# Optimization experiments

Measured on AMD Instinct MI355X. Metric: run time of the kernel, lower is better.

## Reference

```python
import jax, jax.numpy as jnp
import numpy as np

N_EMB = 1024
HEAD_SIZE = 64
BLOCK_SIZE = 2048
B, T = 8, 2048


def setup_inputs() -> dict:
    key = jax.random.key(0)
    kx, kq, kk, kv = jax.random.split(key, 4)
    scale = 1.0 / (N_EMB ** 0.5)
    x = jax.random.normal(kx, (B, T, N_EMB), dtype=jnp.float32)
    Wq = jax.random.uniform(kq, (N_EMB, HEAD_SIZE), dtype=jnp.float32) * scale
    Wk = jax.random.uniform(kk, (N_EMB, HEAD_SIZE), dtype=jnp.float32) * scale
    Wv = jax.random.uniform(kv, (N_EMB, HEAD_SIZE), dtype=jnp.float32) * scale
    return {"x": x, "Wq": Wq, "Wk": Wk, "Wv": Wv}


def reference(x, Wq, Wk, Wv):
    # Faithful to Head.__call__ with is_training=False.
    # NOTE: original code applies NO 1/sqrt(head_size) scaling to the scores.
    Bt, Tt, _ = x.shape
    q = x @ Wq                      # (B, T, H)
    k = x @ Wk                      # (B, T, H)
    v = x @ Wv                      # (B, T, H)
    wei = jnp.einsum('bth,bsh->bts', q, k)  # (B, T, T)
    causal = jnp.tril(jnp.ones((Tt, Tt), dtype=bool))
    wei = jnp.where(causal, wei, -jnp.inf)
    wei = jax.nn.softmax(wei, axis=-1)
    out = jnp.einsum('bts,bsh->bth', wei, v)  # (B, T, H)
    return out
```

## Files before the change

### kernel.cpp

```cpp
#include <hip/hip_runtime.h>
#include <hip/hip_bf16.h>

#define BB 8
#define TT 2048
#define EE 1024
#define HH 64

typedef __attribute__((ext_vector_type(8))) short short8;
typedef __attribute__((ext_vector_type(4))) float f32x4;

__device__ inline f32x4 mfma_16x16x32(short8 a, short8 b, f32x4 c) {
  return __builtin_amdgcn_mfma_f32_16x16x32_bf16(a, b, c, 0, 0, 0);
}

__device__ inline void gload_lds16(const __hip_bfloat16* g, __hip_bfloat16* l) {
  __builtin_amdgcn_global_load_lds((const __attribute__((address_space(1))) void*)g,
                                   (__attribute__((address_space(3))) void*)l,
                                   16, 0, 0);
}

__device__ inline short f2bf(float f) {
  __hip_bfloat16 h = __float2bfloat16(f);
  return *reinterpret_cast<short*>(&h);
}
__device__ inline float bf2f(short s) {
  __hip_bfloat16 h = *reinterpret_cast<__hip_bfloat16*>(&s);
  return __bfloat162float(h);
}

#define WAIT_LGKM0() __builtin_amdgcn_s_waitcnt(0xC07F)

__global__ void prep_w(const float* __restrict__ Wq, const float* __restrict__ Wk,
                       const float* __restrict__ Wv,
                       __hip_bfloat16* __restrict__ Wthi,
                       __hip_bfloat16* __restrict__ Wtlo) {
  const int n = blockIdx.x;
  const int m = n >> 6;
  const int h = n & 63;
  const float* W = (m == 0) ? Wq : (m == 1) ? Wk : Wv;
  const int e0 = threadIdx.x * 4;
#pragma unroll
  for (int j = 0; j < 4; ++j) {
    const float w = W[(e0 + j) * 64 + h];
    const __hip_bfloat16 hi = __float2bfloat16(w);
    Wthi[n * 1024 + e0 + j] = hi;
    Wtlo[n * 1024 + e0 + j] = __float2bfloat16(w - __bfloat162float(hi));
  }
}

__global__ __launch_bounds__(256) void qkv_gemm(
    const float* __restrict__ x,
    const __hip_bfloat16* __restrict__ Wthi, const __hip_bfloat16* __restrict__ Wtlo,
    __hip_bfloat16* __restrict__ qhi, __hip_bfloat16* __restrict__ qlo,
    __hip_bfloat16* __restrict__ khi, __hip_bfloat16* __restrict__ klo,
    __hip_bfloat16* __restrict__ vT) {
  __shared__ __hip_bfloat16 Ahi[2][64 * 72];
  __shared__ __hip_bfloat16 Alo[2][64 * 72];
  __shared__ __hip_bfloat16 Bhi[2][192 * 64];
  __shared__ __hip_bfloat16 Blo[2][128 * 64];

  const int tid  = threadIdx.x;
  const int wave = tid >> 6;
  const int lane = tid & 63;
  const int row0 = blockIdx.x * 64;

  const int lr = tid >> 2;
  const int le = (tid & 3) * 16;
  const float* xrow = x + (row0 + lr) * 1024 + le;

  f32x4 acc[12];
#pragma unroll
  for (int j = 0; j < 12; ++j) acc[j] = f32x4{0.f, 0.f, 0.f, 0.f};

  const int l15 = lane & 15, l4 = lane >> 4;

  auto issue_B = [&](int c, int buf) {
    const int g = (lane & 7) ^ ((lane >> 3) & 7);
#pragma unroll
    for (int s = 0; s < 6; ++s) {
      const int qq = wave * 6 + s;
      const int n  = qq * 8 + (lane >> 3);
      gload_lds16(Wthi + n * 1024 + c * 64 + g * 8, &Bhi[buf][qq * 512]);
      if (qq < 16)
        gload_lds16(Wtlo + n * 1024 + c * 64 + g * 8, &Blo[buf][qq * 512]);
    }
  };
  auto write_A = [&](int buf, const f32x4* xr) {
    short8 h0, h1, l0, l1;
    const float* xf = (const float*)xr;
#pragma unroll
    for (int j = 0; j < 8; ++j) {
      const float v = xf[j];
      const short h = f2bf(v);
      h0[j] = h;
      l0[j] = f2bf(v - bf2f(h));
    }
#pragma unroll
    for (int j = 0; j < 8; ++j) {
      const float v = xf[8 + j];
      const short h = f2bf(v);
      h1[j] = h;
      l1[j] = f2bf(v - bf2f(h));
    }
    *(short8*)&Ahi[buf][lr * 72 + le]     = h0;
    *(short8*)&Ahi[buf][lr * 72 + le + 8] = h1;
    *(short8*)&Alo[buf][lr * 72 + le]     = l0;
    *(short8*)&Alo[buf][lr * 72 + le + 8] = l1;
  };
  auto compute = [&](int buf) {
    const int tr = wave * 16 + l15;
    short8 ah0 = *(const short8*)&Ahi[buf][tr * 72 + l4 * 8];
    short8 ah1 = *(const short8*)&Ahi[buf][tr * 72 + 32 + l4 * 8];
    short8 al0 = *(const short8*)&Alo[buf][tr * 72 + l4 * 8];
    short8 al1 = *(const short8*)&Alo[buf][tr * 72 + 32 + l4 * 8];
#pragma unroll
    for (int j = 0; j < 12; ++j) {
      const int n  = j * 16 + l15;
      const int o0 = ((l4)     ^ (n & 7)) * 8;
      const int o1 = ((4 + l4) ^ (n & 7)) * 8;
      short8 bh0 = *(const short8*)&Bhi[buf][n * 64 + o0];
      short8 bh1 = *(const short8*)&Bhi[buf][n * 64 + o1];
      acc[j] = mfma_16x16x32(ah0, bh0, acc[j]);
      acc[j] = mfma_16x16x32(ah1, bh1, acc[j]);
      if (j < 8) {
        short8 bl0 = *(const short8*)&Blo[buf][n * 64 + o0];
        short8 bl1 = *(const short8*)&Blo[buf][n * 64 + o1];
        acc[j] = mfma_16x16x32(ah0, bl0, acc[j]);
        acc[j] = mfma_16x16x32(ah1, bl1, acc[j]);
        acc[j] = mfma_16x16x32(al0, bh0, acc[j]);
        acc[j] = mfma_16x16x32(al1, bh1, acc[j]);
      }
    }
  };

  f32x4 xr[4], xn[4];
  {
    const f32x4* p = (const f32x4*)xrow;
    xr[0] = p[0]; xr[1] = p[1]; xr[2] = p[2]; xr[3] = p[3];
  }
  issue_B(0, 0);
  __builtin_amdgcn_s_waitcnt(0);
  write_A(0, xr);
  __syncthreads();

  for (int c = 0; c < 16; ++c) {
    const int p = c & 1;
    if (c < 15) {
      const f32x4* pp = (const f32x4*)(xrow + (c + 1) * 64);
      xn[0] = pp[0]; xn[1] = pp[1]; xn[2] = pp[2]; xn[3] = pp[3];
      issue_B(c + 1, p ^ 1);
    }
    compute(p);
    if (c < 15) {
      __builtin_amdgcn_s_waitcnt(0);
      write_A(p ^ 1, xn);
    }
    __syncthreads();
  }

  const int strip = wave * 16;
#pragma unroll
  for (int j = 0; j < 12; ++j) {
    const int n  = j * 16 + l15;
    const int mm = n >> 6;
    const int h  = n & 63;
#pragma unroll
    for (int r = 0; r < 4; ++r) {
      const int trow = row0 + strip + l4 * 4 + r;
      const float val = acc[j][r];
      const __hip_bfloat16 hi = __float2bfloat16(val);
      const __hip_bfloat16 lo = __float2bfloat16(val - __bfloat162float(hi));
      if (mm == 0) {
        qhi[trow * 64 + h] = hi;
        qlo[trow * 64 + h] = lo;
      } else if (mm == 1) {
        khi[trow * 64 + h] = hi;
        klo[trow * 64 + h] = lo;
      } else {
        const int bb = trow >> 11, tl = trow & 2047;
        vT[(bb * 64 + h) * 2048 + tl] = hi;
      }
    }
  }
}

__global__ __launch_bounds__(256, 2) void attn(
    const __hip_bfloat16* __restrict__ qhi, const __hip_bfloat16* __restrict__ qlo,
    const __hip_bfloat16* __restrict__ khi, const __hip_bfloat16* __restrict__ klo,
    const __hip_bfloat16* __restrict__ vT, float* __restrict__ out) {
  __shared__ __hip_bfloat16 Psm[4][2][16 * 72];
  __shared__ float Osm[4][32][65];
  __shared__ float Msm[4][32];
  __shared__ float Lsm[4][32];

  const int tid  = threadIdx.x;
  const int wave = tid >> 6;
  const int lane = tid & 63;
  const int l15 = lane & 15, l4 = lane >> 4;

  const int b  = blockIdx.x & 7;
  const int ss = 63 - (blockIdx.x >> 3);
  const int t0 = ss * 32;
  const int ntiles = (ss >> 1) + 1;

  short8 qh0[2], qh1[2], ql0[2], ql1[2];
#pragma unroll
  for (int m = 0; m < 2; ++m) {
    const __hip_bfloat16* qph = qhi + (b * 2048 + t0 + m * 16 + l15) * 64;
    const __hip_bfloat16* qpl = qlo + (b * 2048 + t0 + m * 16 + l15) * 64;
    qh0[m] = *(const short8*)(qph + l4 * 8);
    qh1[m] = *(const short8*)(qph + 32 + l4 * 8);
    ql0[m] = *(const short8*)(qpl + l4 * 8);
    ql1[m] = *(const short8*)(qpl + 32 + l4 * 8);
  }

  f32x4 acc[2][4];
#pragma unroll
  for (int m = 0; m < 2; ++m)
#pragma unroll
    for (int j = 0; j < 4; ++j) acc[m][j] = f32x4{0.f, 0.f, 0.f, 0.f};
  float m_[2][4], l_[2][4];
#pragma unroll
  for (int m = 0; m < 2; ++m)
#pragma unroll
    for (int r = 0; r < 4; ++r) { m_[m][r] = -1e30f; l_[m][r] = 0.f; }

  const __hip_bfloat16* kbase_h = khi + (size_t)b * 2048 * 64;
  const __hip_bfloat16* kbase_l = klo + (size_t)b * 2048 * 64;
  const __hip_bfloat16* vbase   = vT + (size_t)b * 64 * 2048;

  for (int kt = wave; kt < ntiles; kt += 4) {
    const int k0 = kt << 6;
    const bool diag = (kt == ntiles - 1);

    short8 kh0[4], kh1[4], kl0[4], kl1[4];
#pragma unroll
    for (int j = 0; j < 4; ++j) {
      const __hip_bfloat16* kph = kbase_h + (k0 + j * 16 + l15) * 64;
      const __hip_bfloat16* kpl = kbase_l + (k0 + j * 16 + l15) * 64;
      kh0[j] = *(const short8*)(kph + l4 * 8);
      kh1[j] = *(const short8*)(kph + 32 + l4 * 8);
      kl0[j] = *(const short8*)(kpl + l4 * 8);
      kl1[j] = *(const short8*)(kpl + 32 + l4 * 8);
    }

#pragma unroll
    for (int m = 0; m < 2; ++m) {
      const int rowbase = t0 + m * 16;
      f32x4 s_[4];
#pragma unroll
      for (int j = 0; j < 4; ++j) {
        if (diag && (k0 + j * 16) > (rowbase + 15)) {
          s_[j] = f32x4{-1e30f, -1e30f, -1e30f, -1e30f};
          continue;
        }
        f32x4 z = f32x4{0.f, 0.f, 0.f, 0.f};
        z = mfma_16x16x32(qh0[m], kh0[j], z);
        z = mfma_16x16x32(qh1[m], kh1[j], z);
        z = mfma_16x16x32(qh0[m], kl0[j], z);
        z = mfma_16x16x32(qh1[m], kl1[j], z);
        z = mfma_16x16x32(ql0[m], kh0[j], z);
        z = mfma_16x16x32(ql1[m], kh1[j], z);
        s_[j] = z;
      }
      if (diag) {
#pragma unroll
        for (int j = 0; j < 4; ++j) {
          const int key = k0 + j * 16 + l15;
#pragma unroll
          for (int r = 0; r < 4; ++r) {
            const int row = rowbase + l4 * 4 + r;
            if (key > row) s_[j][r] = -1e30f;
          }
        }
      }

      float mx[4], rs[4], al[4];
#pragma unroll
      for (int r = 0; r < 4; ++r)
        mx[r] = fmaxf(fmaxf(s_[0][r], s_[1][r]), fmaxf(s_[2][r], s_[3][r]));
      for (int off = 1; off < 16; off <<= 1) {
#pragma unroll
        for (int r = 0; r < 4; ++r) mx[r] = fmaxf(mx[r], __shfl_xor(mx[r], off));
      }
#pragma unroll
      for (int r = 0; r < 4; ++r) {
        const float mn = fmaxf(m_[m][r], mx[r]);
        al[r] = __expf(m_[m][r] - mn);
        m_[m][r] = mn;
        rs[r] = 0.f;
      }
#pragma unroll
      for (int j = 0; j < 4; ++j) {
#pragma unroll
        for (int r = 0; r < 4; ++r) {
          const float pv = __expf(s_[j][r] - m_[m][r]);
          s_[j][r] = pv;
          rs[r] += pv;
        }
      }
      for (int off = 1; off < 16; off <<= 1) {
#pragma unroll
        for (int r = 0; r < 4; ++r) rs[r] += __shfl_xor(rs[r], off);
      }
#pragma unroll
      for (int r = 0; r < 4; ++r) l_[m][r] = l_[m][r] * al[r] + rs[r];
#pragma unroll
      for (int j = 0; j < 4; ++j)
#pragma unroll
        for (int r = 0; r < 4; ++r) acc[m][j][r] *= al[r];

#pragma unroll
      for (int j = 0; j < 4; ++j)
#pragma unroll
        for (int r = 0; r < 4; ++r)
          Psm[wave][m][(l4 * 4 + r) * 72 + j * 16 + l15] =
              __float2bfloat16(s_[j][r]);
    }

    short8 vf0[4], vf1[4];
#pragma unroll
    for (int j = 0; j < 4; ++j) {
      const __hip_bfloat16* vp = vbase + (j * 16 + l15) * 2048 + k0;
      vf0[j] = *(const short8*)(vp + l4 * 8);
      vf1[j] = *(const short8*)(vp + 32 + l4 * 8);
    }

    WAIT_LGKM0();

#pragma unroll
    for (int m = 0; m < 2; ++m) {
      short8 pf0 = *(const short8*)&Psm[wave][m][l15 * 72 + l4 * 8];
      short8 pf1 = *(const short8*)&Psm[wave][m][l15 * 72 + 32 + l4 * 8];
#pragma unroll
      for (int j = 0; j < 4; ++j) {
        acc[m][j] = mfma_16x16x32(pf0, vf0[j], acc[m][j]);
        acc[m][j] = mfma_16x16x32(pf1, vf1[j], acc[m][j]);
      }
    }
  }

#pragma unroll
  for (int m = 0; m < 2; ++m) {
#pragma unroll
    for (int j = 0; j < 4; ++j)
#pragma unroll
      for (int r = 0; r < 4; ++r)
        Osm[wave][m * 16 + l4 * 4 + r][j * 16 + l15] = acc[m][j][r];
    if (l15 == 0) {
#pragma unroll
      for (int r = 0; r < 4; ++r) {
        Msm[wave][m * 16 + l4 * 4 + r] = m_[m][r];
        Lsm[wave][m * 16 + l4 * 4 + r] = l_[m][r];
      }
    }
  }
  __syncthreads();

#pragma unroll
  for (int rr = 0; rr < 8; ++rr) {
    const int row = wave * 8 + rr;
    float M = fmaxf(fmaxf(Msm[0][row], Msm[1][row]),
                    fmaxf(Msm[2][row], Msm[3][row]));
    float L = 0.f, O = 0.f;
#pragma unroll
    for (int w2 = 0; w2 < 4; ++w2) {
      const float a = __expf(Msm[w2][row] - M);
      L += a * Lsm[w2][row];
      O += a * Osm[w2][row][lane];
    }
    out[(b * 2048 + t0 + row) * 64 + lane] = O / L;
  }
}

extern "C" void kernel_launch(void* const* d_in, const int* in_sizes, int n_in,
                              void* d_out, int out_size, void* d_ws, size_t ws_size,
                              hipStream_t stream) {
  const float* x  = (const float*)d_in[0];
  const float* Wq = (const float*)d_in[1];
  const float* Wk = (const float*)d_in[2];
  const float* Wv = (const float*)d_in[3];
  float* out = (float*)d_out;

  char* ws = (char*)d_ws;
  __hip_bfloat16* Wthi = (__hip_bfloat16*)ws;
  __hip_bfloat16* Wtlo = (__hip_bfloat16*)(ws + 393216);
  __hip_bfloat16* qhi  = (__hip_bfloat16*)(ws + 786432);
  __hip_bfloat16* qlo  = (__hip_bfloat16*)(ws + 786432 + 1 * 2097152);
  __hip_bfloat16* khi  = (__hip_bfloat16*)(ws + 786432 + 2 * 2097152);
  __hip_bfloat16* klo  = (__hip_bfloat16*)(ws + 786432 + 3 * 2097152);
  __hip_bfloat16* vT   = (__hip_bfloat16*)(ws + 786432 + 4 * 2097152);

  prep_w<<<192, 256, 0, stream>>>(Wq, Wk, Wv, Wthi, Wtlo);
  qkv_gemm<<<256, 256, 0, stream>>>(x, Wthi, Wtlo, qhi, qlo, khi, klo, vT);
  attn<<<512, 256, 0, stream>>>(qhi, qlo, khi, klo, vT, out);
}
```

Measured before the change: 161.0 us.

## Halve per-block row tiles in QKV GEMM and attention to double grid parallelism

The QKV GEMM now processes 32 rows per block with waves split over output columns, and loads the low-part W fragments directly into registers instead of LDS. This doubles the grid to 512 blocks. The attention kernel handles 16 query rows per block instead of 32, doubling its grid to 1024 and raising the occupancy hint to 4. The aim is better load balance and occupancy across the many CUs, at the cost of reloading K/V tiles more often and doing less reuse per block.

```diff
diff --git a/kernel.cpp b/kernel.cpp
--- a/kernel.cpp
+++ b/kernel.cpp
@@ -54,39 +54,50 @@
     __hip_bfloat16* __restrict__ qhi, __hip_bfloat16* __restrict__ qlo,
     __hip_bfloat16* __restrict__ khi, __hip_bfloat16* __restrict__ klo,
     __hip_bfloat16* __restrict__ vT) {
-  __shared__ __hip_bfloat16 Ahi[2][64 * 72];
-  __shared__ __hip_bfloat16 Alo[2][64 * 72];
+  __shared__ __hip_bfloat16 Ahi[2][32 * 72];
+  __shared__ __hip_bfloat16 Alo[2][32 * 72];
   __shared__ __hip_bfloat16 Bhi[2][192 * 64];
-  __shared__ __hip_bfloat16 Blo[2][128 * 64];
 
   const int tid  = threadIdx.x;
   const int wave = tid >> 6;
   const int lane = tid & 63;
-  const int row0 = blockIdx.x * 64;
-
-  const int lr = tid >> 2;
-  const int le = (tid & 3) * 16;
+  const int row0 = blockIdx.x * 32;
+  const int l15 = lane & 15, l4 = lane >> 4;
+
+  const int lr = tid >> 3;
+  const int le = (tid & 7) * 8;
   const float* xrow = x + (row0 + lr) * 1024 + le;
 
-  f32x4 acc[12];
-#pragma unroll
-  for (int j = 0; j < 12; ++j) acc[j] = f32x4{0.f, 0.f, 0.f, 0.f};
-
-  const int l15 = lane & 15, l4 = lane >> 4;
-
-  auto issue_B = [&](int c, int buf) {
+  f32x4 acc[2][3];
+#pragma unroll
+  for (int m = 0; m < 2; ++m)
+#pragma unroll
+    for (int j = 0; j < 3; ++j) acc[m][j] = f32x4{0.f, 0.f, 0.f, 0.f};
+
+  auto issue_Bhi = [&](int c, int buf) {
     const int g = (lane & 7) ^ ((lane >> 3) & 7);
 #pragma unroll
-    for (int s = 0; s < 6; ++s) {
-      const int qq = wave * 6 + s;
-      const int n  = qq * 8 + (lane >> 3);
-      gload_lds16(Wthi + n * 1024 + c * 64 + g * 8, &Bhi[buf][qq * 512]);
-      if (qq < 16)
-        gload_lds16(Wtlo + n * 1024 + c * 64 + g * 8, &Blo[buf][qq * 512]);
+    for (int s = 0; s < 3; ++s) {
+      const int j = wave + s * 4;
+#pragma unroll
+      for (int qh = 0; qh < 2; ++qh) {
+        const int qq = j * 2 + qh;
+        const int n  = qq * 8 + (lane >> 3);
+        gload_lds16(Wthi + n * 1024 + c * 64 + g * 8, &Bhi[buf][qq * 512]);
+      }
+    }
+  };
+  auto load_Blo = [&](int c, short8* bl) {
+#pragma unroll
+    for (int jj = 0; jj < 2; ++jj) {
+      const int j = wave + jj * 4;
+      const __hip_bfloat16* p = Wtlo + (j * 16 + l15) * 1024 + c * 64;
+      bl[jj * 2]     = *(const short8*)(p + l4 * 8);
+      bl[jj * 2 + 1] = *(const short8*)(p + 32 + l4 * 8);
     }
   };
   auto write_A = [&](int buf, const f32x4* xr) {
-    short8 h0, h1, l0, l1;
+    short8 h0, l0;
     const float* xf = (const float*)xr;
 #pragma unroll
     for (int j = 0; j < 8; ++j) {
@@ -95,50 +106,45 @@
       h0[j] = h;
       l0[j] = f2bf(v - bf2f(h));
     }
-#pragma unroll
-    for (int j = 0; j < 8; ++j) {
-      const float v = xf[8 + j];
-      const short h = f2bf(v);
-      h1[j] = h;
-      l1[j] = f2bf(v - bf2f(h));
-    }
-    *(short8*)&Ahi[buf][lr * 72 + le]     = h0;
-    *(short8*)&Ahi[buf][lr * 72 + le + 8] = h1;
-    *(short8*)&Alo[buf][lr * 72 + le]     = l0;
-    *(short8*)&Alo[buf][lr * 72 + le + 8] = l1;
+    *(short8*)&Ahi[buf][lr * 72 + le] = h0;
+    *(short8*)&Alo[buf][lr * 72 + le] = l0;
   };
-  auto compute = [&](int buf) {
-    const int tr = wave * 16 + l15;
-    short8 ah0 = *(const short8*)&Ahi[buf][tr * 72 + l4 * 8];
-    short8 ah1 = *(const short8*)&Ahi[buf][tr * 72 + 32 + l4 * 8];
-    short8 al0 = *(const short8*)&Alo[buf][tr * 72 + l4 * 8];
-    short8 al1 = *(const short8*)&Alo[buf][tr * 72 + 32 + l4 * 8];
-#pragma unroll
-    for (int j = 0; j < 12; ++j) {
-      const int n  = j * 16 + l15;
-      const int o0 = ((l4)     ^ (n & 7)) * 8;
-      const int o1 = ((4 + l4) ^ (n & 7)) * 8;
-      short8 bh0 = *(const short8*)&Bhi[buf][n * 64 + o0];
-      short8 bh1 = *(const short8*)&Bhi[buf][n * 64 + o1];
-      acc[j] = mfma_16x16x32(ah0, bh0, acc[j]);
-      acc[j] = mfma_16x16x32(ah1, bh1, acc[j]);
-      if (j < 8) {
-        short8 bl0 = *(const short8*)&Blo[buf][n * 64 + o0];
-        short8 bl1 = *(const short8*)&Blo[buf][n * 64 + o1];
-        acc[j] = mfma_16x16x32(ah0, bl0, acc[j]);
-        acc[j] = mfma_16x16x32(ah1, bl1, acc[j]);
-        acc[j] = mfma_16x16x32(al0, bh0, acc[j]);
-        acc[j] = mfma_16x16x32(al1, bh1, acc[j]);
+  auto compute = [&](int buf, const short8* bl) {
+#pragma unroll
+    for (int m = 0; m < 2; ++m) {
+      const int tr = m * 16 + l15;
+      short8 ah0 = *(const short8*)&Ahi[buf][tr * 72 + l4 * 8];
+      short8 ah1 = *(const short8*)&Ahi[buf][tr * 72 + 32 + l4 * 8];
+      short8 al0 = *(const short8*)&Alo[buf][tr * 72 + l4 * 8];
+      short8 al1 = *(const short8*)&Alo[buf][tr * 72 + 32 + l4 * 8];
+#pragma unroll
+      for (int jj = 0; jj < 3; ++jj) {
+        const int j  = (jj < 2) ? (wave + jj * 4) : (wave + 8);
+        const int n  = j * 16 + l15;
+        const int o0 = ((l4)     ^ (n & 7)) * 8;
+        const int o1 = ((4 + l4) ^ (n & 7)) * 8;
+        short8 bh0 = *(const short8*)&Bhi[buf][n * 64 + o0];
+        short8 bh1 = *(const short8*)&Bhi[buf][n * 64 + o1];
+        acc[m][jj] = mfma_16x16x32(ah0, bh0, acc[m][jj]);
+        acc[m][jj] = mfma_16x16x32(ah1, bh1, acc[m][jj]);
+        if (jj < 2) {
+          acc[m][jj] = mfma_16x16x32(ah0, bl[jj * 2],     acc[m][jj]);
+          acc[m][jj] = mfma_16x16x32(ah1, bl[jj * 2 + 1], acc[m][jj]);
+          acc[m][jj] = mfma_16x16x32(al0, bh0, acc[m][jj]);
+          acc[m][jj] = mfma_16x16x32(al1, bh1, acc[m][jj]);
+        }
       }
     }
   };
 
-  f32x4 xr[4], xn[4];
+  f32x4 xr[2], xn[2];
   {
     const f32x4* p = (const f32x4*)xrow;
-    xr[0] = p[0]; xr[1] = p[1]; xr[2] = p[2]; xr[3] = p[3];
-  }
-  issue_B(0, 0);
+    xr[0] = p[0]; xr[1] = p[1];
+  }
+  short8 blc[4], bln[4];
+  issue_Bhi(0, 0);
+  load_Blo(0, blc);
   __builtin_amdgcn_s_waitcnt(0);
   write_A(0, xr);
   __syncthreads();
@@ -147,51 +153,54 @@
     const int p = c & 1;
     if (c < 15) {
       const f32x4* pp = (const f32x4*)(xrow + (c + 1) * 64);
-      xn[0] = pp[0]; xn[1] = pp[1]; xn[2] = pp[2]; xn[3] = pp[3];
-      issue_B(c + 1, p ^ 1);
-    }
-    compute(p);
+      xn[0] = pp[0]; xn[1] = pp[1];
+      issue_Bhi(c + 1, p ^ 1);
+      load_Blo(c + 1, bln);
+    }
+    compute(p, blc);
     if (c < 15) {
       __builtin_amdgcn_s_waitcnt(0);
       write_A(p ^ 1, xn);
+#pragma unroll
+      for (int q = 0; q < 4; ++q) blc[q] = bln[q];
     }
     __syncthreads();
   }
 
-  const int strip = wave * 16;
-#pragma unroll
-  for (int j = 0; j < 12; ++j) {
-    const int n  = j * 16 + l15;
-    const int mm = n >> 6;
-    const int h  = n & 63;
-#pragma unroll
-    for (int r = 0; r < 4; ++r) {
-      const int trow = row0 + strip + l4 * 4 + r;
-      const float val = acc[j][r];
-      const __hip_bfloat16 hi = __float2bfloat16(val);
-      const __hip_bfloat16 lo = __float2bfloat16(val - __bfloat162float(hi));
-      if (mm == 0) {
-        qhi[trow * 64 + h] = hi;
-        qlo[trow * 64 + h] = lo;
-      } else if (mm == 1) {
-        khi[trow * 64 + h] = hi;
-        klo[trow * 64 + h] = lo;
-      } else {
-        const int bb = trow >> 11, tl = trow & 2047;
-        vT[(bb * 64 + h) * 2048 + tl] = hi;
-      }
-    }
-  }
-}
-
-__global__ __launch_bounds__(256, 2) void attn(
+  const int hcol = wave * 16 + l15;
+#pragma unroll
+  for (int jj = 0; jj < 3; ++jj) {
+#pragma unroll
+    for (int m = 0; m < 2; ++m) {
+#pragma unroll
+      for (int r = 0; r < 4; ++r) {
+        const int trow = row0 + m * 16 + l4 * 4 + r;
+        const float val = acc[m][jj][r];
+        if (jj == 0) {
+          const __hip_bfloat16 hi = __float2bfloat16(val);
+          qhi[trow * 64 + hcol] = hi;
+          qlo[trow * 64 + hcol] = __float2bfloat16(val - __bfloat162float(hi));
+        } else if (jj == 1) {
+          const __hip_bfloat16 hi = __float2bfloat16(val);
+          khi[trow * 64 + hcol] = hi;
+          klo[trow * 64 + hcol] = __float2bfloat16(val - __bfloat162float(hi));
+        } else {
+          const int bb = trow >> 11, tl = trow & 2047;
+          vT[(bb * 64 + hcol) * 2048 + tl] = __float2bfloat16(val);
+        }
+      }
+    }
+  }
+}
+
+__global__ __launch_bounds__(256, 4) void attn(
     const __hip_bfloat16* __restrict__ qhi, const __hip_bfloat16* __restrict__ qlo,
     const __hip_bfloat16* __restrict__ khi, const __hip_bfloat16* __restrict__ klo,
     const __hip_bfloat16* __restrict__ vT, float* __restrict__ out) {
-  __shared__ __hip_bfloat16 Psm[4][2][16 * 72];
-  __shared__ float Osm[4][32][65];
-  __shared__ float Msm[4][32];
-  __shared__ float Lsm[4][32];
+  __shared__ __hip_bfloat16 Psm[4][16 * 72];
+  __shared__ float Osm[4][16][65];
+  __shared__ float Msm[4][16];
+  __shared__ float Lsm[4][16];
 
   const int tid  = threadIdx.x;
   const int wave = tid >> 6;
@@ -199,31 +208,23 @@
   const int l15 = lane & 15, l4 = lane >> 4;
 
   const int b  = blockIdx.x & 7;
-  const int ss = 63 - (blockIdx.x >> 3);
-  const int t0 = ss * 32;
-  const int ntiles = (ss >> 1) + 1;
-
-  short8 qh0[2], qh1[2], ql0[2], ql1[2];
-#pragma unroll
-  for (int m = 0; m < 2; ++m) {
-    const __hip_bfloat16* qph = qhi + (b * 2048 + t0 + m * 16 + l15) * 64;
-    const __hip_bfloat16* qpl = qlo + (b * 2048 + t0 + m * 16 + l15) * 64;
-    qh0[m] = *(const short8*)(qph + l4 * 8);
-    qh1[m] = *(const short8*)(qph + 32 + l4 * 8);
-    ql0[m] = *(const short8*)(qpl + l4 * 8);
-    ql1[m] = *(const short8*)(qpl + 32 + l4 * 8);
-  }
-
-  f32x4 acc[2][4];
-#pragma unroll
-  for (int m = 0; m < 2; ++m)
-#pragma unroll
-    for (int j = 0; j < 4; ++j) acc[m][j] = f32x4{0.f, 0.f, 0.f, 0.f};
-  float m_[2][4], l_[2][4];
-#pragma unroll
-  for (int m = 0; m < 2; ++m)
-#pragma unroll
-    for (int r = 0; r < 4; ++r) { m_[m][r] = -1e30f; l_[m][r] = 0.f; }
+  const int ss = 127 - (blockIdx.x >> 3);
+  const int t0 = ss * 16;
+  const int ntiles = (ss >> 2) + 1;
+
+  const __hip_bfloat16* qph = qhi + (b * 2048 + t0 + l15) * 64;
+  const __hip_bfloat16* qpl = qlo + (b * 2048 + t0 + l15) * 64;
+  const short8 qh0 = *(const short8*)(qph + l4 * 8);
+  const short8 qh1 = *(const short8*)(qph + 32 + l4 * 8);
+  const short8 ql0 = *(const short8*)(qpl + l4 * 8);
+  const short8 ql1 = *(const short8*)(qpl + 32 + l4 * 8);
+
+  f32x4 acc[4];
+#pragma unroll
+  for (int j = 0; j < 4; ++j) acc[j] = f32x4{0.f, 0.f, 0.f, 0.f};
+  float m_[4], l_[4];
+#pragma unroll
+  for (int r = 0; r < 4; ++r) { m_[r] = -1e30f; l_[r] = 0.f; }
 
   const __hip_bfloat16* kbase_h = khi + (size_t)b * 2048 * 64;
   const __hip_bfloat16* kbase_l = klo + (size_t)b * 2048 * 64;
@@ -233,90 +234,80 @@
     const int k0 = kt << 6;
     const bool diag = (kt == ntiles - 1);
 
-    short8 kh0[4], kh1[4], kl0[4], kl1[4];
+    f32x4 s_[4];
 #pragma unroll
     for (int j = 0; j < 4; ++j) {
-      const __hip_bfloat16* kph = kbase_h + (k0 + j * 16 + l15) * 64;
-      const __hip_bfloat16* kpl = kbase_l + (k0 + j * 16 + l15) * 64;
-      kh0[j] = *(const short8*)(kph + l4 * 8);
-      kh1[j] = *(const short8*)(kph + 32 + l4 * 8);
-      kl0[j] = *(const short8*)(kpl + l4 * 8);
-      kl1[j] = *(const short8*)(kpl + 32 + l4 * 8);
-    }
-
-#pragma unroll
-    for (int m = 0; m < 2; ++m) {
-      const int rowbase = t0 + m * 16;
-      f32x4 s_[4];
+      if (diag && (k0 + j * 16) > (t0 + 15)) {
+        s_[j] = f32x4{-1e30f, -1e30f, -1e30f, -1e30f};
+      } else {
+        const __hip_bfloat16* kph = kbase_h + (k0 + j * 16 + l15) * 64;
+        const __hip_bfloat16* kpl = kbase_l + (k0 + j * 16 + l15) * 64;
+        const short8 kh0 = *(const short8*)(kph + l4 * 8);
+        const short8 kh1 = *(const short8*)(kph + 32 + l4 * 8);
+        const short8 kl0 = *(const short8*)(kpl + l4 * 8);
+        const short8 kl1 = *(const short8*)(kpl + 32 + l4 * 8);
+        f32x4 z = f32x4{0.f, 0.f, 0.f, 0.f};
+        z = mfma_16x16x32(qh0, kh0, z);
+        z = mfma_16x16x32(qh1, kh1, z);
+        z = mfma_16x16x32(qh0, kl0, z);
+        z = mfma_16x16x32(qh1, kl1, z);
+        z = mfma_16x16x32(ql0, kh0, z);
+        z = mfma_16x16x32(ql1, kh1, z);
+        s_[j] = z;
+      }
+    }
+    if (diag) {
 #pragma unroll
       for (int j = 0; j < 4; ++j) {
-        if (diag && (k0 + j * 16) > (rowbase + 15)) {
-          s_[j] = f32x4{-1e30f, -1e30f, -1e30f, -1e30f};
-          continue;
+        const int key = k0 + j * 16 + l15;
+#pragma unroll
+        for (int r = 0; r < 4; ++r) {
+          const int row = t0 + l4 * 4 + r;
+          if (key > row) s_[j][r] = -1e30f;
         }
-        f32x4 z = f32x4{0.f, 0.f, 0.f, 0.f};
-        z = mfma_16x16x32(qh0[m], kh0[j], z);
-        z = mfma_16x16x32(qh1[m], kh1[j], z);
-        z = mfma_16x16x32(qh0[m], kl0[j], z);
-        z = mfma_16x16x32(qh1[m], kl1[j], z);
-        z = mfma_16x16x32(ql0[m], kh0[j], z);
-        z = mfma_16x16x32(ql1[m], kh1[j], z);
-        s_[j] = z;
-      }
-      if (diag) {
-#pragma unroll
-        for (int j = 0; j < 4; ++j) {
-          const int key = k0 + j * 16 + l15;
-#pragma unroll
-          for (int r = 0; r < 4; ++r) {
-            const int row = rowbase + l4 * 4 + r;
-            if (key > row) s_[j][r] = -1e30f;
-          }
-        }
-      }
-
-      float mx[4], rs[4], al[4];
+      }
+    }
+
+    float mx[4], rs[4], al[4];
+#pragma unroll
+    for (int r = 0; r < 4; ++r)
+      mx[r] = fmaxf(fmaxf(s_[0][r], s_[1][r]), fmaxf(s_[2][r], s_[3][r]));
+    for (int off = 1; off < 16; off <<= 1) {
+#pragma unroll
+      for (int r = 0; r < 4; ++r) mx[r] = fmaxf(mx[r], __shfl_xor(mx[r], off));
+    }
+#pragma unroll
+    for (int r = 0; r < 4; ++r) {
+      const float mn = fmaxf(m_[r], mx[r]);
+      al[r] = __expf(m_[r] - mn);
+      m_[r] = mn;
+      rs[r] = 0.f;
+    }
+#pragma unroll
+    for (int j = 0; j < 4; ++j) {
+#pragma unroll
+      for (int r = 0; r < 4; ++r) {
+        const float pv = __expf(s_[j][r] - m_[r]);
+        s_[j][r] = pv;
+        rs[r] += pv;
+      }
+    }
+    for (int off = 1; off < 16; off <<= 1) {
+#pragma unroll
+      for (int r = 0; r < 4; ++r) rs[r] += __shfl_xor(rs[r], off);
+    }
+#pragma unroll
+    for (int r = 0; r < 4; ++r) l_[r] = l_[r] * al[r] + rs[r];
+#pragma unroll
+    for (int j = 0; j < 4; ++j)
+#pragma unroll
+      for (int r = 0; r < 4; ++r) acc[j][r] *= al[r];
+
+#pragma unroll
+    for (int j = 0; j < 4; ++j)
 #pragma unroll
       for (int r = 0; r < 4; ++r)
-        mx[r] = fmaxf(fmaxf(s_[0][r], s_[1][r]), fmaxf(s_[2][r], s_[3][r]));
-      for (int off = 1; off < 16; off <<= 1) {
-#pragma unroll
-        for (int r = 0; r < 4; ++r) mx[r] = fmaxf(mx[r], __shfl_xor(mx[r], off));
-      }
-#pragma unroll
-      for (int r = 0; r < 4; ++r) {
-        const float mn = fmaxf(m_[m][r], mx[r]);
-        al[r] = __expf(m_[m][r] - mn);
-        m_[m][r] = mn;
-        rs[r] = 0.f;
-      }
-#pragma unroll
-      for (int j = 0; j < 4; ++j) {
-#pragma unroll
-        for (int r = 0; r < 4; ++r) {
-          const float pv = __expf(s_[j][r] - m_[m][r]);
-          s_[j][r] = pv;
-          rs[r] += pv;
-        }
-      }
-      for (int off = 1; off < 16; off <<= 1) {
-#pragma unroll
-        for (int r = 0; r < 4; ++r) rs[r] += __shfl_xor(rs[r], off);
-      }
-#pragma unroll
-      for (int r = 0; r < 4; ++r) l_[m][r] = l_[m][r] * al[r] + rs[r];
-#pragma unroll
-      for (int j = 0; j < 4; ++j)
-#pragma unroll
-        for (int r = 0; r < 4; ++r) acc[m][j][r] *= al[r];
-
-#pragma unroll
-      for (int j = 0; j < 4; ++j)
-#pragma unroll
-        for (int r = 0; r < 4; ++r)
-          Psm[wave][m][(l4 * 4 + r) * 72 + j * 16 + l15] =
-              __float2bfloat16(s_[j][r]);
-    }
+        Psm[wave][(l4 * 4 + r) * 72 + j * 16 + l15] = __float2bfloat16(s_[j][r]);
 
     short8 vf0[4], vf1[4];
 #pragma unroll
@@ -328,38 +319,32 @@
 
     WAIT_LGKM0();
 
-#pragma unroll
-    for (int m = 0; m < 2; ++m) {
-      short8 pf0 = *(const short8*)&Psm[wave][m][l15 * 72 + l4 * 8];
-      short8 pf1 = *(const short8*)&Psm[wave][m][l15 * 72 + 32 + l4 * 8];
-#pragma unroll
-      for (int j = 0; j < 4; ++j) {
-        acc[m][j] = mfma_16x16x32(pf0, vf0[j], acc[m][j]);
-        acc[m][j] = mfma_16x16x32(pf1, vf1[j], acc[m][j]);
-      }
-    }
-  }
-
-#pragma unroll
-  for (int m = 0; m < 2; ++m) {
-#pragma unroll
-    for (int j = 0; j < 4; ++j)
-#pragma unroll
-      for (int r = 0; r < 4; ++r)
-        Osm[wave][m * 16 + l4 * 4 + r][j * 16 + l15] = acc[m][j][r];
-    if (l15 == 0) {
-#pragma unroll
-      for (int r = 0; r < 4; ++r) {
-        Msm[wave][m * 16 + l4 * 4 + r] = m_[m][r];
-        Lsm[wave][m * 16 + l4 * 4 + r] = l_[m][r];
-      }
+    const short8 pf0 = *(const short8*)&Psm[wave][l15 * 72 + l4 * 8];
+    const short8 pf1 = *(const short8*)&Psm[wave][l15 * 72 + 32 + l4 * 8];
+#pragma unroll
+    for (int j = 0; j < 4; ++j) {
+      acc[j] = mfma_16x16x32(pf0, vf0[j], acc[j]);
+      acc[j] = mfma_16x16x32(pf1, vf1[j], acc[j]);
+    }
+  }
+
+#pragma unroll
+  for (int j = 0; j < 4; ++j)
+#pragma unroll
+    for (int r = 0; r < 4; ++r)
+      Osm[wave][l4 * 4 + r][j * 16 + l15] = acc[j][r];
+  if (l15 == 0) {
+#pragma unroll
+    for (int r = 0; r < 4; ++r) {
+      Msm[wave][l4 * 4 + r] = m_[r];
+      Lsm[wave][l4 * 4 + r] = l_[r];
     }
   }
   __syncthreads();
 
 #pragma unroll
-  for (int rr = 0; rr < 8; ++rr) {
-    const int row = wave * 8 + rr;
+  for (int rr = 0; rr < 4; ++rr) {
+    const int row = wave * 4 + rr;
     float M = fmaxf(fmaxf(Msm[0][row], Msm[1][row]),
                     fmaxf(Msm[2][row], Msm[3][row]));
     float L = 0.f, O = 0.f;
@@ -392,6 +377,6 @@
   __hip_bfloat16* vT   = (__hip_bfloat16*)(ws + 786432 + 4 * 2097152);
 
   prep_w<<<192, 256, 0, stream>>>(Wq, Wk, Wv, Wthi, Wtlo);
-  qkv_gemm<<<256, 256, 0, stream>>>(x, Wthi, Wtlo, qhi, qlo, khi, klo, vT);
-  attn<<<512, 256, 0, stream>>>(qhi, qlo, khi, klo, vT, out);
-}
+  qkv_gemm<<<512, 256, 0, stream>>>(x, Wthi, Wtlo, qhi, qlo, khi, klo, vT);
+  attn<<<1024, 256, 0, stream>>>(qhi, qlo, khi, klo, vT, out);
+}
```

Result: slower. 183.0 us (+13.6%).
